# Kernel optimization log

Measured on AMD Instinct MI355X. Metric: run time of the kernel, lower is better.

Reference implementation:

```python
import jax, jax.numpy as jnp
import numpy as np

B, E, S, H = 8, 1024, 2048, 16  # batch, embed_dim, seq_len, n_heads
D = E // H                       # per-head hidden dim


def setup_inputs() -> dict:
    key = jax.random.key(0)
    k1, k2 = jax.random.split(key)
    x = jax.random.normal(k1, (B, E, S), dtype=jnp.float32)
    weight = jax.random.normal(k2, (H, S), dtype=jnp.float32)  # nn.Parameter(torch.randn)
    bias = jnp.zeros((H, S), dtype=jnp.float32)                # nn.Parameter(torch.zeros)
    return {"x": x, "weight": weight, "bias": bias}


def _vector_to_matrix(v):
    # v: (H, S) -> M: (H, S, S), M[h, i, j] = v[h, j - i] if j >= i else 0
    h, m = v.shape
    i = jnp.arange(m)[:, None]
    j = jnp.arange(m)[None, :]
    off = j - i  # negative offsets wrap (same as torch fancy indexing) but are masked out
    return jnp.where(j >= i, v[:, off], jnp.zeros((), dtype=v.dtype))


def reference(x, weight, bias):
    b, e, s = x.shape
    h = weight.shape[0]
    d = e // h
    M = _vector_to_matrix(weight)  # (H, S, S)
    # Original: x.view(B,H,D,S).reshape(B*H,D,S) paired with W.repeat_interleave(B,0),
    # i.e. flat index k uses M[k // B]. Group the flat B*H axis into H contiguous
    # blocks of size B so each block shares one Toeplitz matrix (no (B*H,S,S) blowup).
    xg = x.reshape(b * h, d, s).reshape(h, b, d, s)  # block m = M[m]
    out = jnp.einsum('mbds,mst->mbdt', xg, M) + bias[:, None, None, :]
    return out.reshape(b, e, s)
```

## Files before the change

kernel.cpp:

```cpp
#include <hip/hip_runtime.h>
#include <hip/hip_bf16.h>

#define SEQ    2048
#define NHEAD  16
#define RPH    512
#define BK     64
#define NTH    256

#define WSTRIDE 2184
#define ABUF_E  2048
#define WCOP_E  (8 * ABUF_E)
#define TOT_E   (WCOP_E + 8 * WSTRIDE)

typedef float  f32x4  __attribute__((ext_vector_type(4)));
typedef __bf16 bf16x8 __attribute__((ext_vector_type(8)));

struct PF { float4 v0, v1; };

__device__ __forceinline__ unsigned f2bf(float f) {
    union { __hip_bfloat16 h; unsigned short u; } cv;
    cv.h = __float2bfloat16(f);
    return (unsigned)cv.u;
}

__device__ __forceinline__ uint4 pack8u(float4 a, float4 b) {
    union { bf16x8 v; uint4 u; } r;
    r.v[0] = (__bf16)a.x; r.v[1] = (__bf16)a.y;
    r.v[2] = (__bf16)a.z; r.v[3] = (__bf16)a.w;
    r.v[4] = (__bf16)b.x; r.v[5] = (__bf16)b.y;
    r.v[6] = (__bf16)b.z; r.v[7] = (__bf16)b.w;
    return r.u;
}

#define MFMA16(a, b, c) __builtin_amdgcn_mfma_f32_16x16x32_bf16((a), (b), (c), 0, 0, 0)

#define LOADPF(P, CH)                                                         \
  { const float* g_ = Xp + (size_t)(CH) * BK;                                 \
    P.v0 = *(const float4*)g_;                                                \
    P.v1 = *(const float4*)(g_ + 4); }

#define WRITEA(AB, P)  { *(uint4*)((AB) + wb0) = pack8u(P.v0, P.v1); }

#define KSTEPQ(ABC, KS, P)                                                    \
  { const int kb_ = (64 * (KS) + kq16) ^ swz;                                 \
    bf16x8 af0 = *(const bf16x8*)((ABC) + Arow0 + kb_);                       \
    bf16x8 af1 = *(const bf16x8*)((ABC) + Arow1 + kb_);                       \
    acc[0][0] = MFMA16(af0, bw[((P)+2*(KS)-0)&15], acc[0][0]);                \
    acc[1][0] = MFMA16(af1, bw[((P)+2*(KS)-0)&15], acc[1][0]);                \
    acc[0][1] = MFMA16(af0, bw[((P)+2*(KS)-1)&15], acc[0][1]);                \
    acc[1][1] = MFMA16(af1, bw[((P)+2*(KS)-1)&15], acc[1][1]);                \
    acc[0][2] = MFMA16(af0, bw[((P)+2*(KS)-2)&15], acc[0][2]);                \
    acc[1][2] = MFMA16(af1, bw[((P)+2*(KS)-2)&15], acc[1][2]);                \
    acc[0][3] = MFMA16(af0, bw[((P)+2*(KS)-3)&15], acc[0][3]);                \
    acc[1][3] = MFMA16(af1, bw[((P)+2*(KS)-3)&15], acc[1][3]);                \
    acc[0][4] = MFMA16(af0, bw[((P)+2*(KS)-4)&15], acc[0][4]);                \
    acc[1][4] = MFMA16(af1, bw[((P)+2*(KS)-4)&15], acc[1][4]);                \
    acc[0][5] = MFMA16(af0, bw[((P)+2*(KS)-5)&15], acc[0][5]);                \
    acc[1][5] = MFMA16(af1, bw[((P)+2*(KS)-5)&15], acc[1][5]);                \
    acc[0][6] = MFMA16(af0, bw[((P)+2*(KS)-6)&15], acc[0][6]);                \
    acc[1][6] = MFMA16(af1, bw[((P)+2*(KS)-6)&15], acc[1][6]);                \
    acc[0][7] = MFMA16(af0, bw[((P)+2*(KS)-7)&15], acc[0][7]);                \
    acc[1][7] = MFMA16(af1, bw[((P)+2*(KS)-7)&15], acc[1][7]); }

#define SUPER(CH, P, C0, C1, N0, N1)                                          \
  {                                                                           \
    if ((CH) < nchw) {                                                        \
      __builtin_amdgcn_s_setprio(1);                                          \
      KSTEPQ(C0, 0, P);                                                       \
      bw[((P)+1)&15] = *(const bf16x8*)(wcB + 64 * (CH) + 16);                \
      bw[((P)+2)&15] = *(const bf16x8*)(wcB + 64 * (CH) + 32);                \
      KSTEPQ(C0, 1, P);                                                       \
      __builtin_amdgcn_s_setprio(0);                                          \
    }                                                                         \
    if ((CH) + 1 < nchw) {                                                    \
      bw[((P)+3)&15] = *(const bf16x8*)(wcB + 64 * (CH) + 48);                \
      bw[((P)+4)&15] = *(const bf16x8*)(wcB + 64 * (CH) + 64);                \
      __builtin_amdgcn_s_setprio(1);                                          \
      KSTEPQ(C1, 0, (P) + 4);                                                 \
      bw[((P)+5)&15] = *(const bf16x8*)(wcB + 64 * (CH) + 80);                \
      bw[((P)+6)&15] = *(const bf16x8*)(wcB + 64 * (CH) + 96);                \
      KSTEPQ(C1, 1, (P) + 4);                                                 \
      __builtin_amdgcn_s_setprio(0);                                          \
    }                                                                         \
    if ((CH) + 2 < nchw) {                                                    \
      bw[((P)+7)&15] = *(const bf16x8*)(wcB + 64 * (CH) + 112);               \
      bw[((P)+8)&15] = *(const bf16x8*)(wcB + 64 * (CH) + 128);               \
    }                                                                         \
    WRITEA(N0, pfA);                            \
    WRITEA(N1, pfB);                            \
    if ((CH) + 6 < nch) LOADPF(pfA, (CH) + 6);                                \
    if ((CH) + 7 < nch) LOADPF(pfB, (CH) + 7);                                \
    asm volatile("s_waitcnt lgkmcnt(2)\n\ts_barrier" ::: "memory");           \
  }

__global__ __launch_bounds__(NTH, 2) void mixer_kernel(
    const float* __restrict__ x, const float* __restrict__ wgt,
    const float* __restrict__ bias, float* __restrict__ out)
{
    __shared__ unsigned short smem[TOT_E] __attribute__((aligned(16)));
    char* b0 = (char*)smem;
    char* b1 = (char*)smem + ABUF_E * 2;
    char* b2 = (char*)smem + ABUF_E * 4;
    char* b3 = (char*)smem + ABUF_E * 6;
    char* b4 = (char*)smem + ABUF_E * 8;
    char* b5 = (char*)smem + ABUF_E * 10;
    char* b6 = (char*)smem + ABUF_E * 12;
    char* b7 = (char*)smem + ABUF_E * 14;
    unsigned short* wc = smem + WCOP_E;

    const int tid  = threadIdx.x;
    const int lane = tid & 63;
    const int tb   = tid >> 6;

    const int bid  = blockIdx.x;
    const int m    = (bid & 7) + 8 * ((bid >> 3) & 1);
    const int rt   = (bid >> 4) & 15;
    const int pc   = bid >> 8;
    const int qA   = pc ? 2 : 3;
    const int qB   = pc ? 1 : 0;

    const float* Xb = x   + (size_t)(m * RPH + rt * 32) * SEQ;
    float*       Ob = out + (size_t)(m * RPH + rt * 32) * SEQ;
    const float* wr = wgt  + m * SEQ;
    const float* br = bias + m * SEQ;

    const int srow = tid >> 3;
    const int wsw  = (srow & 7) << 4;
    const int wb0  = srow * 128 + (((tid & 7) * 16) ^ wsw);
    const float* Xp = Xb + (size_t)srow * SEQ + (tid & 7) * 8;

    PF pfA, pfB;
    LOADPF(pfA, 0);
    LOADPF(pfB, 1);

    {
        const int t8 = tid * 8;
        const float* g = wr + (2040 - t8);
        float4 lo = *(const float4*)g;
        float4 hi = *(const float4*)(g + 4);
        uint4 v;
        v.x = f2bf(hi.w) | (f2bf(hi.z) << 16);
        v.y = f2bf(hi.y) | (f2bf(hi.x) << 16);
        v.z = f2bf(lo.w) | (f2bf(lo.z) << 16);
        v.w = f2bf(lo.y) | (f2bf(lo.x) << 16);
        *(uint4*)(smem + 8 + t8) = v;
        if (tid < 21) {
            uint4 z = {0u, 0u, 0u, 0u};
            unsigned short* dst = (tid == 0) ? smem
                                 : smem + 8 + 2048 + (tid - 1) * 8;
            *(uint4*)dst = z;
        }
    }
    __syncthreads();

    #pragma unroll
    for (int c = 0; c < 8; ++c) {
        for (int grp = tid; grp < WSTRIDE / 8; grp += NTH) {
            const int i = grp * 8;
            uint4 g0 = *(const uint4*)(smem + 8 + i - 8);
            uint4 g1 = *(const uint4*)(smem + 8 + i);
            unsigned d[9] = {g0.x, g0.y, g0.z, g0.w,
                             g1.x, g1.y, g1.z, g1.w, 0u};
            const int qd = (16 - 2 * c) >> 2;
            uint4 o;
            if (c & 1) {
                o.x = (d[qd]     >> 16) | (d[qd + 1] << 16);
                o.y = (d[qd + 1] >> 16) | (d[qd + 2] << 16);
                o.z = (d[qd + 2] >> 16) | (d[qd + 3] << 16);
                o.w = (d[qd + 3] >> 16) | (d[qd + 4] << 16);
            } else {
                o.x = d[qd];     o.y = d[qd + 1];
                o.z = d[qd + 2]; o.w = d[qd + 3];
            }
            *(uint4*)(wc + c * WSTRIDE + i) = o;
        }
    }
    __syncthreads();

    const int col_low = lane & 15;
    const int kq      = lane >> 4;
    const int kq16    = kq * 16;
    const int swz     = (col_low & 7) << 4;
    const int cpy     = (col_low + 1) & 7;
    const int BcBase  = cpy * WSTRIDE + cpy + 2047 - col_low + 8 * kq;
    const int Arow0   = col_low * 128;
    const int Arow1   = (col_low + 16) * 128;

    for (int h = 0; h < 2; ++h) {
        const int q    = h ? qB : qA;
        const int nch  = 8 * q + 8;
        const int nchw = 8 * q + 2 * tb + 2;
        const int t0w  = 512 * q + 128 * tb;
        const unsigned short* wcB = wc + (BcBase - t0w);

        if (h) { LOADPF(pfA, 0); LOADPF(pfB, 1); }

        bf16x8 bw[16];
        #pragma unroll
        for (int w = -7; w <= 0; ++w)
            bw[w & 15] = *(const bf16x8*)(wcB + 16 * w);

        WRITEA(b0, pfA);
        WRITEA(b1, pfB);
        LOADPF(pfA, 2);
        LOADPF(pfB, 3);
        WRITEA(b2, pfA);
        WRITEA(b3, pfB);
        LOADPF(pfA, 4);
        LOADPF(pfB, 5);
        asm volatile("s_waitcnt lgkmcnt(0)\n\ts_barrier" ::: "memory");

        f32x4 acc[2][8] = {};
        for (int ch = 0; ch < nch; ch += 8) {
            SUPER(ch,     0, b0, b1, b4, b5);
            SUPER(ch + 2, 8, b2, b3, b6, b7);
            SUPER(ch + 4, 0, b4, b5, b0, b1);
            SUPER(ch + 6, 8, b6, b7, b2, b3);
        }

        #pragma unroll
        for (int c = 0; c < 8; ++c) {
            const int colg = t0w + 16 * c + col_low;
            const float bv = br[colg];
            #pragma unroll
            for (int a = 0; a < 2; ++a) {
                const int rowl = 16 * a + 4 * kq;
                #pragma unroll
                for (int rr = 0; rr < 4; ++rr)
                    Ob[(size_t)(rowl + rr) * SEQ + colg] = acc[a][c][rr] + bv;
            }
        }
    }
}

extern "C" void kernel_launch(void* const* d_in, const int* in_sizes, int n_in,
                              void* d_out, int out_size, void* d_ws, size_t ws_size,
                              hipStream_t stream) {
    const float* x  = (const float*)d_in[0];
    const float* w  = (const float*)d_in[1];
    const float* bs = (const float*)d_in[2];
    float* out = (float*)d_out;
    dim3 grid(512);
    dim3 block(NTH);
    hipLaunchKernelGGL(mixer_kernel, grid, block, 0, stream, x, w, bs, out);
}
```

Baseline: 41.05 us.

## Switch Toeplitz GEMM inner loop from 16x16x32 to 32x32x16 MFMA tiles

New measurement: 43.50 us. 1.06x slower.

```diff
diff --git a/kernel.cpp b/kernel.cpp
--- a/kernel.cpp
+++ b/kernel.cpp
@@ -12,7 +12,7 @@
 #define WCOP_E  (8 * ABUF_E)
 #define TOT_E   (WCOP_E + 8 * WSTRIDE)
 
-typedef float  f32x4  __attribute__((ext_vector_type(4)));
+typedef float  f32x16 __attribute__((ext_vector_type(16)));
 typedef __bf16 bf16x8 __attribute__((ext_vector_type(8)));
 
 struct PF { float4 v0, v1; };
@@ -32,7 +32,7 @@
     return r.u;
 }
 
-#define MFMA16(a, b, c) __builtin_amdgcn_mfma_f32_16x16x32_bf16((a), (b), (c), 0, 0, 0)
+#define MFMA32(a, b, c) __builtin_amdgcn_mfma_f32_32x32x16_bf16((a), (b), (c), 0, 0, 0)
 
 #define LOADPF(P, CH)                                                         \
   { const float* g_ = Xp + (size_t)(CH) * BK;                                 \
@@ -41,50 +41,40 @@
 
 #define WRITEA(AB, P)  { *(uint4*)((AB) + wb0) = pack8u(P.v0, P.v1); }
 
-#define KSTEPQ(ABC, KS, P)                                                    \
-  { const int kb_ = (64 * (KS) + kq16) ^ swz;                                 \
-    bf16x8 af0 = *(const bf16x8*)((ABC) + Arow0 + kb_);                       \
-    bf16x8 af1 = *(const bf16x8*)((ABC) + Arow1 + kb_);                       \
-    acc[0][0] = MFMA16(af0, bw[((P)+2*(KS)-0)&15], acc[0][0]);                \
-    acc[1][0] = MFMA16(af1, bw[((P)+2*(KS)-0)&15], acc[1][0]);                \
-    acc[0][1] = MFMA16(af0, bw[((P)+2*(KS)-1)&15], acc[0][1]);                \
-    acc[1][1] = MFMA16(af1, bw[((P)+2*(KS)-1)&15], acc[1][1]);                \
-    acc[0][2] = MFMA16(af0, bw[((P)+2*(KS)-2)&15], acc[0][2]);                \
-    acc[1][2] = MFMA16(af1, bw[((P)+2*(KS)-2)&15], acc[1][2]);                \
-    acc[0][3] = MFMA16(af0, bw[((P)+2*(KS)-3)&15], acc[0][3]);                \
-    acc[1][3] = MFMA16(af1, bw[((P)+2*(KS)-3)&15], acc[1][3]);                \
-    acc[0][4] = MFMA16(af0, bw[((P)+2*(KS)-4)&15], acc[0][4]);                \
-    acc[1][4] = MFMA16(af1, bw[((P)+2*(KS)-4)&15], acc[1][4]);                \
-    acc[0][5] = MFMA16(af0, bw[((P)+2*(KS)-5)&15], acc[0][5]);                \
-    acc[1][5] = MFMA16(af1, bw[((P)+2*(KS)-5)&15], acc[1][5]);                \
-    acc[0][6] = MFMA16(af0, bw[((P)+2*(KS)-6)&15], acc[0][6]);                \
-    acc[1][6] = MFMA16(af1, bw[((P)+2*(KS)-6)&15], acc[1][6]);                \
-    acc[0][7] = MFMA16(af0, bw[((P)+2*(KS)-7)&15], acc[0][7]);                \
-    acc[1][7] = MFMA16(af1, bw[((P)+2*(KS)-7)&15], acc[1][7]); }
+#define KSTEP32(ABC, KS, P)                                                   \
+  { bf16x8 af = *(const bf16x8*)((ABC) + ArowA + ((32 * (KS) + kq16) ^ swz)); \
+    acc[0] = MFMA32(af, bw[((P)+(KS)-0)&15], acc[0]);                         \
+    acc[1] = MFMA32(af, bw[((P)+(KS)-2)&15], acc[1]);                         \
+    acc[2] = MFMA32(af, bw[((P)+(KS)-4)&15], acc[2]);                         \
+    acc[3] = MFMA32(af, bw[((P)+(KS)-6)&15], acc[3]); }
 
 #define SUPER(CH, P, C0, C1, N0, N1)                                          \
   {                                                                           \
     if ((CH) < nchw) {                                                        \
       __builtin_amdgcn_s_setprio(1);                                          \
-      KSTEPQ(C0, 0, P);                                                       \
-      bw[((P)+1)&15] = *(const bf16x8*)(wcB + 64 * (CH) + 16);                \
-      bw[((P)+2)&15] = *(const bf16x8*)(wcB + 64 * (CH) + 32);                \
-      KSTEPQ(C0, 1, P);                                                       \
+      KSTEP32(C0, 0, P);                                                      \
+      KSTEP32(C0, 1, P);                                                      \
+      KSTEP32(C0, 2, P);                                                      \
+      KSTEP32(C0, 3, P);                                                      \
       __builtin_amdgcn_s_setprio(0);                                          \
     }                                                                         \
     if ((CH) + 1 < nchw) {                                                    \
-      bw[((P)+3)&15] = *(const bf16x8*)(wcB + 64 * (CH) + 48);                \
       bw[((P)+4)&15] = *(const bf16x8*)(wcB + 64 * (CH) + 64);                \
-      __builtin_amdgcn_s_setprio(1);                                          \
-      KSTEPQ(C1, 0, (P) + 4);                                                 \
       bw[((P)+5)&15] = *(const bf16x8*)(wcB + 64 * (CH) + 80);                \
       bw[((P)+6)&15] = *(const bf16x8*)(wcB + 64 * (CH) + 96);                \
-      KSTEPQ(C1, 1, (P) + 4);                                                 \
+      bw[((P)+7)&15] = *(const bf16x8*)(wcB + 64 * (CH) + 112);               \
+      __builtin_amdgcn_s_setprio(1);                                          \
+      KSTEP32(C1, 0, (P) + 4);                                                \
+      KSTEP32(C1, 1, (P) + 4);                                                \
+      KSTEP32(C1, 2, (P) + 4);                                                \
+      KSTEP32(C1, 3, (P) + 4);                                                \
       __builtin_amdgcn_s_setprio(0);                                          \
     }                                                                         \
     if ((CH) + 2 < nchw) {                                                    \
-      bw[((P)+7)&15] = *(const bf16x8*)(wcB + 64 * (CH) + 112);               \
-      bw[((P)+8)&15] = *(const bf16x8*)(wcB + 64 * (CH) + 128);               \
+      bw[((P)+8)&15]  = *(const bf16x8*)(wcB + 64 * (CH) + 128);              \
+      bw[((P)+9)&15]  = *(const bf16x8*)(wcB + 64 * (CH) + 144);              \
+      bw[((P)+10)&15] = *(const bf16x8*)(wcB + 64 * (CH) + 160);              \
+      bw[((P)+11)&15] = *(const bf16x8*)(wcB + 64 * (CH) + 176);              \
     }                                                                         \
     WRITEA(N0, pfA);                            \
     WRITEA(N1, pfB);                            \
@@ -177,14 +167,13 @@
     }
     __syncthreads();
 
-    const int col_low = lane & 15;
-    const int kq      = lane >> 4;
-    const int kq16    = kq * 16;
-    const int swz     = (col_low & 7) << 4;
+    const int col_low = lane & 31;
+    const int kq2     = lane >> 5;
+    const int kq16    = kq2 * 16;
+    const int swz     = (lane & 7) << 4;
     const int cpy     = (col_low + 1) & 7;
-    const int BcBase  = cpy * WSTRIDE + cpy + 2047 - col_low + 8 * kq;
-    const int Arow0   = col_low * 128;
-    const int Arow1   = (col_low + 16) * 128;
+    const int BcBase  = cpy * WSTRIDE + cpy + 2047 - col_low + 8 * kq2;
+    const int ArowA   = col_low * 128;
 
     for (int h = 0; h < 2; ++h) {
         const int q    = h ? qB : qA;
@@ -197,7 +186,7 @@
 
         bf16x8 bw[16];
         #pragma unroll
-        for (int w = -7; w <= 0; ++w)
+        for (int w = -6; w <= 3; ++w)
             bw[w & 15] = *(const bf16x8*)(wcB + 16 * w);
 
         WRITEA(b0, pfA);
@@ -210,7 +199,7 @@
         LOADPF(pfB, 5);
         asm volatile("s_waitcnt lgkmcnt(0)\n\ts_barrier" ::: "memory");
 
-        f32x4 acc[2][8] = {};
+        f32x16 acc[4] = {};
         for (int ch = 0; ch < nch; ch += 8) {
             SUPER(ch,     0, b0, b1, b4, b5);
             SUPER(ch + 2, 8, b2, b3, b6, b7);
@@ -219,15 +208,13 @@
         }
 
         #pragma unroll
-        for (int c = 0; c < 8; ++c) {
-            const int colg = t0w + 16 * c + col_low;
+        for (int c = 0; c < 4; ++c) {
+            const int colg = t0w + 32 * c + col_low;
             const float bv = br[colg];
             #pragma unroll
-            for (int a = 0; a < 2; ++a) {
-                const int rowl = 16 * a + 4 * kq;
-                #pragma unroll
-                for (int rr = 0; rr < 4; ++rr)
-                    Ob[(size_t)(rowl + rr) * SEQ + colg] = acc[a][c][rr] + bv;
+            for (int reg = 0; reg < 16; ++reg) {
+                const int row = (reg & 3) + 8 * (reg >> 2) + 4 * kq2;
+                Ob[(size_t)row * SEQ + colg] = acc[c][reg] + bv;
             }
         }
     }
```

## Split block into two wave groups over 16-row tiles with dedicated stager waves

Applied to the files above, without the earlier changes.

Result: slower. 45.77 us, median of 2 (+11.5%).

```diff
diff --git a/kernel.cpp b/kernel.cpp
--- a/kernel.cpp
+++ b/kernel.cpp
@@ -5,12 +5,12 @@
 #define NHEAD  16
 #define RPH    512
 #define BK     64
-#define NTH    256
+#define NTH    512
 
 #define WSTRIDE 2184
-#define ABUF_E  2048
+#define ABUF_E  1024
 #define WCOP_E  (8 * ABUF_E)
-#define TOT_E   (WCOP_E + 8 * WSTRIDE)
+#define TOT_E   (WCOP_E + 8 * WSTRIDE + 128)
 
 typedef float  f32x4  __attribute__((ext_vector_type(4)));
 typedef __bf16 bf16x8 __attribute__((ext_vector_type(8)));
@@ -41,59 +41,61 @@
 
 #define WRITEA(AB, P)  { *(uint4*)((AB) + wb0) = pack8u(P.v0, P.v1); }
 
-#define KSTEPQ(ABC, KS, P)                                                    \
-  { const int kb_ = (64 * (KS) + kq16) ^ swz;                                 \
-    bf16x8 af0 = *(const bf16x8*)((ABC) + Arow0 + kb_);                       \
-    bf16x8 af1 = *(const bf16x8*)((ABC) + Arow1 + kb_);                       \
-    acc[0][0] = MFMA16(af0, bw[((P)+2*(KS)-0)&15], acc[0][0]);                \
-    acc[1][0] = MFMA16(af1, bw[((P)+2*(KS)-0)&15], acc[1][0]);                \
-    acc[0][1] = MFMA16(af0, bw[((P)+2*(KS)-1)&15], acc[0][1]);                \
-    acc[1][1] = MFMA16(af1, bw[((P)+2*(KS)-1)&15], acc[1][1]);                \
-    acc[0][2] = MFMA16(af0, bw[((P)+2*(KS)-2)&15], acc[0][2]);                \
-    acc[1][2] = MFMA16(af1, bw[((P)+2*(KS)-2)&15], acc[1][2]);                \
-    acc[0][3] = MFMA16(af0, bw[((P)+2*(KS)-3)&15], acc[0][3]);                \
-    acc[1][3] = MFMA16(af1, bw[((P)+2*(KS)-3)&15], acc[1][3]);                \
-    acc[0][4] = MFMA16(af0, bw[((P)+2*(KS)-4)&15], acc[0][4]);                \
-    acc[1][4] = MFMA16(af1, bw[((P)+2*(KS)-4)&15], acc[1][4]);                \
-    acc[0][5] = MFMA16(af0, bw[((P)+2*(KS)-5)&15], acc[0][5]);                \
-    acc[1][5] = MFMA16(af1, bw[((P)+2*(KS)-5)&15], acc[1][5]);                \
-    acc[0][6] = MFMA16(af0, bw[((P)+2*(KS)-6)&15], acc[0][6]);                \
-    acc[1][6] = MFMA16(af1, bw[((P)+2*(KS)-6)&15], acc[1][6]);                \
-    acc[0][7] = MFMA16(af0, bw[((P)+2*(KS)-7)&15], acc[0][7]);                \
-    acc[1][7] = MFMA16(af1, bw[((P)+2*(KS)-7)&15], acc[1][7]); }
-
-#define SUPER(CH, P, C0, C1, N0, N1)                                          \
+#define KSTEP0(ABC)                                                           \
+  { bf16x8 af = *(const bf16x8*)((ABC) + Arow0 + (kq16 ^ swz));               \
+    acc[0] = MFMA16(af, bw[7], acc[0]);                                       \
+    acc[1] = MFMA16(af, bw[6], acc[1]);                                       \
+    acc[2] = MFMA16(af, bw[5], acc[2]);                                       \
+    acc[3] = MFMA16(af, bw[4], acc[3]);                                       \
+    acc[4] = MFMA16(af, bw[3], acc[4]);                                       \
+    acc[5] = MFMA16(af, bw[2], acc[5]);                                       \
+    acc[6] = MFMA16(af, bw[1], acc[6]);                                       \
+    acc[7] = MFMA16(af, bw[0], acc[7]); }
+
+#define KSTEP1(ABC)                                                           \
+  { bf16x8 af = *(const bf16x8*)((ABC) + Arow0 + ((64 + kq16) ^ swz));        \
+    acc[7] = MFMA16(af, bw[2], acc[7]);                                       \
+    acc[6] = MFMA16(af, bw[3], acc[6]);                                       \
+    acc[5] = MFMA16(af, bw[4], acc[5]);                                       \
+    acc[4] = MFMA16(af, bw[5], acc[4]);                                       \
+    acc[3] = MFMA16(af, bw[6], acc[3]);                                       \
+    acc[2] = MFMA16(af, bw[7], acc[2]);                                       \
+    acc[1] = MFMA16(af, bw[0], acc[1]);                                       \
+    acc[0] = MFMA16(af, bw[1], acc[0]); }
+
+#define CHUNKM(CH, ABC)                                                       \
+  if ((CH) < nchw) {                                                          \
+    const unsigned short* bq_ = wcB + 64 * (CH) - 112;                        \
+    bw[0] = *(const bf16x8*)(bq_);                                            \
+    bw[1] = *(const bf16x8*)(bq_ + 16);                                       \
+    bw[2] = *(const bf16x8*)(bq_ + 32);                                       \
+    bw[3] = *(const bf16x8*)(bq_ + 48);                                       \
+    bw[4] = *(const bf16x8*)(bq_ + 64);                                       \
+    bw[5] = *(const bf16x8*)(bq_ + 80);                                       \
+    bw[6] = *(const bf16x8*)(bq_ + 96);                                       \
+    bw[7] = *(const bf16x8*)(bq_ + 112);                                      \
+    __builtin_amdgcn_s_setprio(1);                                            \
+    KSTEP0(ABC);                                                              \
+    bw[0] = *(const bf16x8*)(bq_ + 128);                          \
+    bw[1] = *(const bf16x8*)(bq_ + 144);                          \
+    KSTEP1(ABC);                                                              \
+    __builtin_amdgcn_s_setprio(0);                                            \
+  }
+
+#define SUPER(CH, C0, C1, N0, N1)                                             \
   {                                                                           \
-    if ((CH) < nchw) {                                                        \
-      __builtin_amdgcn_s_setprio(1);                                          \
-      KSTEPQ(C0, 0, P);                                                       \
-      bw[((P)+1)&15] = *(const bf16x8*)(wcB + 64 * (CH) + 16);                \
-      bw[((P)+2)&15] = *(const bf16x8*)(wcB + 64 * (CH) + 32);                \
-      KSTEPQ(C0, 1, P);                                                       \
-      __builtin_amdgcn_s_setprio(0);                                          \
+    CHUNKM(CH, C0);                                                           \
+    CHUNKM((CH) + 1, C1);                                                     \
+    if (stager) {                                                             \
+      WRITEA(N0, pfA);                          \
+      WRITEA(N1, pfB);                          \
+      if ((CH) + 6 < nch) LOADPF(pfA, (CH) + 6);                              \
+      if ((CH) + 7 < nch) LOADPF(pfB, (CH) + 7);                              \
     }                                                                         \
-    if ((CH) + 1 < nchw) {                                                    \
-      bw[((P)+3)&15] = *(const bf16x8*)(wcB + 64 * (CH) + 48);                \
-      bw[((P)+4)&15] = *(const bf16x8*)(wcB + 64 * (CH) + 64);                \
-      __builtin_amdgcn_s_setprio(1);                                          \
-      KSTEPQ(C1, 0, (P) + 4);                                                 \
-      bw[((P)+5)&15] = *(const bf16x8*)(wcB + 64 * (CH) + 80);                \
-      bw[((P)+6)&15] = *(const bf16x8*)(wcB + 64 * (CH) + 96);                \
-      KSTEPQ(C1, 1, (P) + 4);                                                 \
-      __builtin_amdgcn_s_setprio(0);                                          \
-    }                                                                         \
-    if ((CH) + 2 < nchw) {                                                    \
-      bw[((P)+7)&15] = *(const bf16x8*)(wcB + 64 * (CH) + 112);               \
-      bw[((P)+8)&15] = *(const bf16x8*)(wcB + 64 * (CH) + 128);               \
-    }                                                                         \
-    WRITEA(N0, pfA);                            \
-    WRITEA(N1, pfB);                            \
-    if ((CH) + 6 < nch) LOADPF(pfA, (CH) + 6);                                \
-    if ((CH) + 7 < nch) LOADPF(pfB, (CH) + 7);                                \
     asm volatile("s_waitcnt lgkmcnt(2)\n\ts_barrier" ::: "memory");           \
   }
 
-__global__ __launch_bounds__(NTH, 2) void mixer_kernel(
+__global__ __launch_bounds__(NTH, 4) void mixer_kernel(
     const float* __restrict__ x, const float* __restrict__ wgt,
     const float* __restrict__ bias, float* __restrict__ out)
 {
@@ -110,17 +112,17 @@
 
     const int tid  = threadIdx.x;
     const int lane = tid & 63;
-    const int tb   = tid >> 6;
+    const int wv   = tid >> 6;
+    const int tb   = wv & 3;
+    const int g    = wv >> 2;
+    const bool stager = (tid < 128);
 
     const int bid  = blockIdx.x;
     const int m    = (bid & 7) + 8 * ((bid >> 3) & 1);
-    const int rt   = (bid >> 4) & 15;
-    const int pc   = bid >> 8;
-    const int qA   = pc ? 2 : 3;
-    const int qB   = pc ? 1 : 0;
-
-    const float* Xb = x   + (size_t)(m * RPH + rt * 32) * SEQ;
-    float*       Ob = out + (size_t)(m * RPH + rt * 32) * SEQ;
+    const int rt   = bid >> 4;
+
+    const float* Xb = x   + (size_t)(m * RPH + rt * 16) * SEQ;
+    float*       Ob = out + (size_t)(m * RPH + rt * 16) * SEQ;
     const float* wr = wgt  + m * SEQ;
     const float* br = bias + m * SEQ;
 
@@ -130,14 +132,13 @@
     const float* Xp = Xb + (size_t)srow * SEQ + (tid & 7) * 8;
 
     PF pfA, pfB;
-    LOADPF(pfA, 0);
-    LOADPF(pfB, 1);
-
-    {
+    if (stager) { LOADPF(pfA, 0); LOADPF(pfB, 1); }
+
+    if (tid < 256) {
         const int t8 = tid * 8;
-        const float* g = wr + (2040 - t8);
-        float4 lo = *(const float4*)g;
-        float4 hi = *(const float4*)(g + 4);
+        const float* gw = wr + (2040 - t8);
+        float4 lo = *(const float4*)gw;
+        float4 hi = *(const float4*)(gw + 4);
         uint4 v;
         v.x = f2bf(hi.w) | (f2bf(hi.z) << 16);
         v.y = f2bf(hi.y) | (f2bf(hi.x) << 16);
@@ -184,38 +185,35 @@
     const int cpy     = (col_low + 1) & 7;
     const int BcBase  = cpy * WSTRIDE + cpy + 2047 - col_low + 8 * kq;
     const int Arow0   = col_low * 128;
-    const int Arow1   = (col_low + 16) * 128;
-
-    for (int h = 0; h < 2; ++h) {
-        const int q    = h ? qB : qA;
-        const int nch  = 8 * q + 8;
+
+    #pragma unroll
+    for (int sw = 0; sw < 2; ++sw) {
+        const int q    = sw ? (g ? 0 : 1) : (g ? 2 : 3);
+        const int nch  = sw ? 16 : 32;
         const int nchw = 8 * q + 2 * tb + 2;
         const int t0w  = 512 * q + 128 * tb;
         const unsigned short* wcB = wc + (BcBase - t0w);
 
-        if (h) { LOADPF(pfA, 0); LOADPF(pfB, 1); }
-
-        bf16x8 bw[16];
-        #pragma unroll
-        for (int w = -7; w <= 0; ++w)
-            bw[w & 15] = *(const bf16x8*)(wcB + 16 * w);
-
-        WRITEA(b0, pfA);
-        WRITEA(b1, pfB);
-        LOADPF(pfA, 2);
-        LOADPF(pfB, 3);
-        WRITEA(b2, pfA);
-        WRITEA(b3, pfB);
-        LOADPF(pfA, 4);
-        LOADPF(pfB, 5);
+        if (stager) {
+            if (sw) { LOADPF(pfA, 0); LOADPF(pfB, 1); }
+            WRITEA(b0, pfA);
+            WRITEA(b1, pfB);
+            LOADPF(pfA, 2);
+            LOADPF(pfB, 3);
+            WRITEA(b2, pfA);
+            WRITEA(b3, pfB);
+            LOADPF(pfA, 4);
+            LOADPF(pfB, 5);
+        }
         asm volatile("s_waitcnt lgkmcnt(0)\n\ts_barrier" ::: "memory");
 
-        f32x4 acc[2][8] = {};
+        bf16x8 bw[8];
+        f32x4 acc[8] = {};
         for (int ch = 0; ch < nch; ch += 8) {
-            SUPER(ch,     0, b0, b1, b4, b5);
-            SUPER(ch + 2, 8, b2, b3, b6, b7);
-            SUPER(ch + 4, 0, b4, b5, b0, b1);
-            SUPER(ch + 6, 8, b6, b7, b2, b3);
+            SUPER(ch,     b0, b1, b4, b5);
+            SUPER(ch + 2, b2, b3, b6, b7);
+            SUPER(ch + 4, b4, b5, b0, b1);
+            SUPER(ch + 6, b6, b7, b2, b3);
         }
 
         #pragma unroll
@@ -223,12 +221,8 @@
             const int colg = t0w + 16 * c + col_low;
             const float bv = br[colg];
             #pragma unroll
-            for (int a = 0; a < 2; ++a) {
-                const int rowl = 16 * a + 4 * kq;
-                #pragma unroll
-                for (int rr = 0; rr < 4; ++rr)
-                    Ob[(size_t)(rowl + rr) * SEQ + colg] = acc[a][c][rr] + bv;
-            }
+            for (int r = 0; r < 4; ++r)
+                Ob[(size_t)(4 * kq + r) * SEQ + colg] = acc[c][r] + bv;
         }
     }
 }
```
